# Kernel optimization log

Measured on AMD Instinct MI355X. Metric: run time of the kernel, lower is better.

Reference implementation:

```python
import jax, jax.numpy as jnp
import numpy as np

TOP_K = 2  # config.num_experts_per_tok


def setup_inputs() -> dict:
    key = jax.random.key(0)
    ks = jax.random.split(key, 5)
    B, S, H, F, E = 1, 2048, 2048, 1408, 8
    sc_h = 1.0 / np.sqrt(H)
    sc_f = 1.0 / np.sqrt(F)
    return {
        "hidden_states": jax.random.normal(ks[0], (B, S, H), jnp.float32),
        "gate_w": jax.random.normal(ks[1], (E, H), jnp.float32) * sc_h,
        "w1": jax.random.normal(ks[2], (E, F, H), jnp.float32) * sc_h,
        "w3": jax.random.normal(ks[3], (E, F, H), jnp.float32) * sc_h,
        "w2": jax.random.normal(ks[4], (E, H, F), jnp.float32) * sc_f,
    }


def reference(hidden_states, gate_w, w1, w3, w2):
    B, S, H = hidden_states.shape
    x = hidden_states.reshape(-1, H)            # [T, H]
    T = x.shape[0]
    E = gate_w.shape[0]

    # Router: logits -> fp32 softmax -> top-k -> renormalize
    router_logits = x @ gate_w.T                # [T, E]
    probs = jax.nn.softmax(router_logits.astype(jnp.float32), axis=-1)
    topk_w, topk_idx = jax.lax.top_k(probs, TOP_K)          # [T, K]
    topk_w = topk_w / topk_w.sum(axis=-1, keepdims=True)
    topk_w = topk_w.astype(x.dtype)

    # Scatter top-k weights into a dense [T, E] combine matrix (zero elsewhere)
    w_full = jnp.zeros((T, E), x.dtype).at[jnp.arange(T)[:, None], topk_idx].add(topk_w)

    # Per-expert SwiGLU MLP applied to all tokens; masked combine honors routing.
    g = jnp.einsum('th,efh->etf', x, w1)        # [E, T, F]
    u = jnp.einsum('th,efh->etf', x, w3)        # [E, T, F]
    h = jax.nn.silu(g) * u                      # [E, T, F]
    y = jnp.einsum('etf,ehf->eth', h, w2)       # [E, T, H]
    out = jnp.einsum('eth,te->th', y, w_full)   # [T, H]

    final_hidden_states = out.reshape(B, S, H)
    return final_hidden_states, router_logits
```

## Files before the change

### kernel.cpp

```cpp
#include <hip/hip_runtime.h>
#include <hip/hip_bf16.h>

#define T_TOK 2048
#define H_DIM 2048
#define F_DIM 1408
#define N_EXP 8
#define BM 128
#define BN 64
#define BK 64

#define NITEM 40
#define G1_NY (F_DIM / BN)
#define G2_NY (H_DIM / BN)
#define G1_CHUNK ((NITEM * G1_NY) / 8)
#define G2_CHUNK ((NITEM * G2_NY) / 8)

typedef float f32x4 __attribute__((ext_vector_type(4)));
typedef short s16x8 __attribute__((ext_vector_type(8)));

#define LOFF(row, kbyte) (((row) << 7) + ((kbyte) ^ (((row) & 7) << 4)))

__device__ __forceinline__ int bf2i(__hip_bfloat162 h) {
  int r; __builtin_memcpy(&r, &h, 4); return r;
}

__device__ __forceinline__ int4 pack8(float4 a, float4 b) {
  int4 r;
  r.x = bf2i(__float22bfloat162_rn(float2{a.x, a.y}));
  r.y = bf2i(__float22bfloat162_rn(float2{a.z, a.w}));
  r.z = bf2i(__float22bfloat162_rn(float2{b.x, b.y}));
  r.w = bf2i(__float22bfloat162_rn(float2{b.z, b.w}));
  return r;
}

__device__ __forceinline__ unsigned short f2bf(float f) {
  __hip_bfloat16 h = __float2bfloat16(f);
  unsigned short r; __builtin_memcpy(&r, &h, 2); return r;
}

__device__ __forceinline__ f32x4 mfma16(s16x8 a, s16x8 b, f32x4 c) {
  return __builtin_amdgcn_mfma_f32_16x16x32_bf16(a, b, c, 0, 0, 0);
}

__global__ void router_kernel(const float* __restrict__ x, const float* __restrict__ gw,
                              float* __restrict__ logits, int* __restrict__ tk_idx,
                              float* __restrict__ tk_w, unsigned short* __restrict__ xb) {
  __shared__ float xs[H_DIM];
  __shared__ float lg[N_EXP];
  const int t = blockIdx.x;
  const int tid = threadIdx.x;
  const float4 xv = ((const float4*)(x + (size_t)t * H_DIM))[tid];
  ((float4*)xs)[tid] = xv;
  int2 cw;
  cw.x = bf2i(__float22bfloat162_rn(float2{xv.x, xv.y}));
  cw.y = bf2i(__float22bfloat162_rn(float2{xv.z, xv.w}));
  ((int2*)(xb + (size_t)t * H_DIM))[tid] = cw;
  __syncthreads();
  const int w = tid >> 6, l = tid & 63;
  const float* g = gw + w * H_DIM;
  float s = 0.f;
  for (int j = l; j < H_DIM; j += 64) s += xs[j] * g[j];
#pragma unroll
  for (int o = 32; o; o >>= 1) s += __shfl_down(s, o);
  if (l == 0) lg[w] = s;
  __syncthreads();
  if (tid == 0) {
    float mx = lg[0];
#pragma unroll
    for (int i = 1; i < N_EXP; i++) mx = fmaxf(mx, lg[i]);
    float p[N_EXP];
#pragma unroll
    for (int i = 0; i < N_EXP; i++) p[i] = __expf(lg[i] - mx);
    int i0 = 0;
#pragma unroll
    for (int i = 1; i < N_EXP; i++) if (p[i] > p[i0]) i0 = i;
    int i1 = (i0 == 0) ? 1 : 0;
#pragma unroll
    for (int i = 0; i < N_EXP; i++) if (i != i0 && p[i] > p[i1]) i1 = i;
    const float ww = p[i0] + p[i1];
    tk_idx[t * 2] = i0; tk_idx[t * 2 + 1] = i1;
    tk_w[t * 2] = p[i0] / ww; tk_w[t * 2 + 1] = p[i1] / ww;
#pragma unroll
    for (int i = 0; i < N_EXP; i++) logits[t * N_EXP + i] = lg[i];
  }
}

__global__ void build_lists(const int* __restrict__ tk_idx, const float* __restrict__ tk_w,
                            int* __restrict__ counts, int* __restrict__ entries,
                            float* __restrict__ wlist) {
  const int e = blockIdx.x;
  const int l = threadIdx.x;
  int base = 0;
  for (int t0 = 0; t0 < T_TOK; t0 += 64) {
    const int t = t0 + l;
    int sel = -1; float w = 0.f;
    const int i0 = tk_idx[t * 2], i1 = tk_idx[t * 2 + 1];
    if (i0 == e) { sel = t * 2; w = tk_w[t * 2]; }
    else if (i1 == e) { sel = t * 2 + 1; w = tk_w[t * 2 + 1]; }
    const unsigned long long mask = __ballot(sel >= 0);
    const int pos = base + __popcll(mask & ((1ull << l) - 1ull));
    if (sel >= 0) { entries[e * T_TOK + pos] = sel; wlist[e * T_TOK + pos] = w; }
    base += __popcll(mask);
  }
  if (l == 0) counts[e] = base;
}

__global__ void build_items(const int* __restrict__ counts, int* __restrict__ items) {
  if (threadIdx.x == 0) {
    int n = 0;
#pragma unroll
    for (int e = 0; e < N_EXP; e++) {
      const int c = counts[e];
      for (int m0 = 0; m0 < c; m0 += BM) items[1 + n++] = (e << 16) | (m0 / BM);
    }
    items[0] = n;
  }
}

#define G1_STEP(VA0, VA1, B10, B11, B30, B31, WA0, WA1, WB10, WB11, WB30, WB31, KNEXT) \
  {                                                                           \
    asm volatile("s_waitcnt lgkmcnt(0)" ::: "memory");                        \
    __builtin_amdgcn_s_barrier();                                             \
    *(int4*)(sAc + offA0) = VA0;                                              \
    *(int4*)(sAc + offA1) = VA1;                                              \
    *(int4*)(sB1c + offB) = pack8(B10, B11);                                  \
    *(int4*)(sB3c + offB) = pack8(B30, B31);                                  \
    const int kn = (KNEXT);                                                   \
    WA0 = *(const int4*)(pa0 + kn);                                           \
    WA1 = *(const int4*)(pa1 + kn);                                           \
    WB10 = *(const float4*)(pb1 + kn);                                        \
    WB11 = *(const float4*)(pb1 + kn + 4);                                    \
    WB30 = *(const float4*)(pb3 + kn);                                        \
    WB31 = *(const float4*)(pb3 + kn + 4);                                    \
    asm volatile("s_waitcnt lgkmcnt(0)" ::: "memory");                        \
    __builtin_amdgcn_s_barrier();                                             \
    _Pragma("unroll")                                                         \
    for (int kk = 0; kk < 2; kk++) {                                          \
      const int kbyte = kk * 64 + kb;                                         \
      const s16x8 a0 = *(const s16x8*)(sAc + LOFF(rowA0, kbyte));             \
      const s16x8 a1 = *(const s16x8*)(sAc + LOFF(rowA1, kbyte));             \
      const s16x8 p0 = *(const s16x8*)(sB1c + LOFF(rowB0, kbyte));            \
      const s16x8 p1 = *(const s16x8*)(sB1c + LOFF(rowB1, kbyte));            \
      const s16x8 q0 = *(const s16x8*)(sB3c + LOFF(rowB0, kbyte));            \
      const s16x8 q1 = *(const s16x8*)(sB3c + LOFF(rowB1, kbyte));            \
      aG[0][0] = mfma16(a0, p0, aG[0][0]); aG[0][1] = mfma16(a0, p1, aG[0][1]); \
      aG[1][0] = mfma16(a1, p0, aG[1][0]); aG[1][1] = mfma16(a1, p1, aG[1][1]); \
      aU[0][0] = mfma16(a0, q0, aU[0][0]); aU[0][1] = mfma16(a0, q1, aU[0][1]); \
      aU[1][0] = mfma16(a1, q0, aU[1][0]); aU[1][1] = mfma16(a1, q1, aU[1][1]); \
    }                                                                         \
  }

__global__ __launch_bounds__(512)
void moe_gemm1(const float* __restrict__ w1, const float* __restrict__ w3,
               const unsigned short* __restrict__ xb,
               const int* __restrict__ counts, const int* __restrict__ entries,
               const int* __restrict__ items,
               unsigned short* __restrict__ hb) {
  const int lin = blockIdx.x;
  const int virt = (lin & 7) * G1_CHUNK + (lin >> 3);
  const int ix = virt % NITEM;
  const int iy = virt / NITEM;
  if (ix >= items[0]) return;
  const int it = items[1 + ix];
  const int e = it >> 16;
  const int m0 = (it & 0xffff) * BM;
  const int cnt = counts[e];
  const int rem = cnt - m0;
  const int n0 = iy * BN;

  __shared__ unsigned short sA[BM * BK];
  __shared__ unsigned short sB1[BN * BK];
  __shared__ unsigned short sB3[BN * BK];
  char* sAc = (char*)sA; char* sB1c = (char*)sB1; char* sB3c = (char*)sB3;

  const int tid = threadIdx.x;
  const int lane = tid & 63;
  const int wave = tid >> 6;
  const int wm = wave >> 1, wn = wave & 1;

  const int* elist = entries + e * T_TOK + m0;

  const int r0 = tid >> 3;
  const int gc = tid & 7;
  const int ra1 = r0 + 64;
  const int tok0 = elist[r0 < rem ? r0 : 0] >> 1;
  const int tok1 = elist[ra1 < rem ? ra1 : 0] >> 1;
  const unsigned short* pa0 = xb + (size_t)tok0 * H_DIM + gc * 8;
  const unsigned short* pa1 = xb + (size_t)tok1 * H_DIM + gc * 8;
  const float* pb1 = w1 + ((size_t)e * F_DIM + n0 + r0) * H_DIM + gc * 8;
  const float* pb3 = w3 + ((size_t)e * F_DIM + n0 + r0) * H_DIM + gc * 8;
  const int offA0 = LOFF(r0, gc * 16);
  const int offA1 = LOFF(ra1, gc * 16);
  const int offB = LOFF(r0, gc * 16);

  const int rowA0 = wm * 32 + (lane & 15);
  const int rowA1 = rowA0 + 16;
  const int rowB0 = wn * 32 + (lane & 15);
  const int rowB1 = rowB0 + 16;
  const int kb = (lane >> 4) * 16;

  const f32x4 zero = {0.f, 0.f, 0.f, 0.f};
  f32x4 aG[2][2], aU[2][2];
#pragma unroll
  for (int i = 0; i < 2; i++)
#pragma unroll
    for (int j = 0; j < 2; j++) { aG[i][j] = zero; aU[i][j] = zero; }

  int4 Pa0 = *(const int4*)(pa0), Pa1 = *(const int4*)(pa1);
  float4 Pb10 = *(const float4*)(pb1), Pb11 = *(const float4*)(pb1 + 4);
  float4 Pb30 = *(const float4*)(pb3), Pb31 = *(const float4*)(pb3 + 4);
  int4 Qa0, Qa1;
  float4 Qb10, Qb11, Qb30, Qb31;

  const int NT1 = H_DIM / BK;
  for (int t = 0; t < NT1; t += 2) {
    const int kq = (t + 1 < NT1) ? (t + 1) * BK : 0;
    const int kp = (t + 2 < NT1) ? (t + 2) * BK : 0;
    G1_STEP(Pa0, Pa1, Pb10, Pb11, Pb30, Pb31, Qa0, Qa1, Qb10, Qb11, Qb30, Qb31, kq);
    G1_STEP(Qa0, Qa1, Qb10, Qb11, Qb30, Qb31, Pa0, Pa1, Pb10, Pb11, Pb30, Pb31, kp);
  }

#pragma unroll
  for (int i = 0; i < 2; i++) {
#pragma unroll
    for (int r = 0; r < 4; r++) {
      const int m = wm * 32 + i * 16 + ((lane >> 4) << 2) + r;
      if (m < rem) {
        const int entry = elist[m];
        unsigned short* hp = hb + (size_t)entry * F_DIM + n0 + wn * 32 + (lane & 15);
#pragma unroll
        for (int j = 0; j < 2; j++) {
          const float g = aG[i][j][r];
          const float u = aU[i][j][r];
          const float s = g / (1.f + __expf(-g)) * u;
          hp[j * 16] = f2bf(s);
        }
      }
    }
  }
}

#define G2_STEP(VA0, VA1, B0, B1, WA0, WA1, WB0, WB1, KNEXT)                  \
  {                                                                           \
    asm volatile("s_waitcnt lgkmcnt(0)" ::: "memory");                        \
    __builtin_amdgcn_s_barrier();                                             \
    *(int4*)(sAc + offA0) = VA0;                                              \
    *(int4*)(sAc + offA1) = VA1;                                              \
    *(int4*)(sBc + offB) = pack8(B0, B1);                                     \
    const int kn = (KNEXT);                                                   \
    WA0 = *(const int4*)(pa0 + kn);                                           \
    WA1 = *(const int4*)(pa1 + kn);                                           \
    WB0 = *(const float4*)(pb + kn);                                          \
    WB1 = *(const float4*)(pb + kn + 4);                                      \
    asm volatile("s_waitcnt lgkmcnt(0)" ::: "memory");                        \
    __builtin_amdgcn_s_barrier();                                             \
    _Pragma("unroll")                                                         \
    for (int kk = 0; kk < 2; kk++) {                                          \
      const int kbyte = kk * 64 + kb;                                         \
      const s16x8 a0 = *(const s16x8*)(sAc + LOFF(rowA0, kbyte));             \
      const s16x8 a1 = *(const s16x8*)(sAc + LOFF(rowA1, kbyte));             \
      const s16x8 f0 = *(const s16x8*)(sBc + LOFF(rowB0, kbyte));             \
      const s16x8 f1 = *(const s16x8*)(sBc + LOFF(rowB1, kbyte));             \
      ac[0][0] = mfma16(a0, f0, ac[0][0]); ac[0][1] = mfma16(a0, f1, ac[0][1]); \
      ac[1][0] = mfma16(a1, f0, ac[1][0]); ac[1][1] = mfma16(a1, f1, ac[1][1]); \
    }                                                                         \
  }

__global__ __launch_bounds__(512)
void moe_gemm2(const float* __restrict__ w2,
               const unsigned short* __restrict__ hb,
               const int* __restrict__ counts, const int* __restrict__ entries,
               const float* __restrict__ wlist, const int* __restrict__ items,
               float* __restrict__ out) {
  const int lin = blockIdx.x;
  const int virt = (lin & 7) * G2_CHUNK + (lin >> 3);
  const int ix = virt % NITEM;
  const int iy = virt / NITEM;
  if (ix >= items[0]) return;
  const int it = items[1 + ix];
  const int e = it >> 16;
  const int m0 = (it & 0xffff) * BM;
  const int cnt = counts[e];
  const int rem = cnt - m0;
  const int n0 = iy * BN;

  __shared__ unsigned short sA[BM * BK];
  __shared__ unsigned short sB[BN * BK];
  char* sAc = (char*)sA; char* sBc = (char*)sB;

  const int tid = threadIdx.x;
  const int lane = tid & 63;
  const int wave = tid >> 6;
  const int wm = wave >> 1, wn = wave & 1;

  const int* elist = entries + e * T_TOK + m0;
  const float* wl = wlist + e * T_TOK + m0;

  const int r0 = tid >> 3;
  const int gc = tid & 7;
  const int ra1 = r0 + 64;
  const int en0 = elist[r0 < rem ? r0 : 0];
  const int en1 = elist[ra1 < rem ? ra1 : 0];
  const unsigned short* pa0 = hb + (size_t)en0 * F_DIM + gc * 8;
  const unsigned short* pa1 = hb + (size_t)en1 * F_DIM + gc * 8;
  const float* pb = w2 + ((size_t)e * H_DIM + n0 + r0) * F_DIM + gc * 8;
  const int offA0 = LOFF(r0, gc * 16);
  const int offA1 = LOFF(ra1, gc * 16);
  const int offB = LOFF(r0, gc * 16);

  const int rowA0 = wm * 32 + (lane & 15);
  const int rowA1 = rowA0 + 16;
  const int rowB0 = wn * 32 + (lane & 15);
  const int rowB1 = rowB0 + 16;
  const int kb = (lane >> 4) * 16;

  const f32x4 zero = {0.f, 0.f, 0.f, 0.f};
  f32x4 ac[2][2];
#pragma unroll
  for (int i = 0; i < 2; i++)
#pragma unroll
    for (int j = 0; j < 2; j++) ac[i][j] = zero;

  int4 Pa0 = *(const int4*)(pa0), Pa1 = *(const int4*)(pa1);
  float4 Pb0 = *(const float4*)(pb), Pb1 = *(const float4*)(pb + 4);
  int4 Qa0, Qa1;
  float4 Qb0, Qb1;

  const int NT2 = F_DIM / BK;
  for (int t = 0; t < NT2; t += 2) {
    const int kq = (t + 1 < NT2) ? (t + 1) * BK : 0;
    const int kp = (t + 2 < NT2) ? (t + 2) * BK : 0;
    G2_STEP(Pa0, Pa1, Pb0, Pb1, Qa0, Qa1, Qb0, Qb1, kq);
    G2_STEP(Qa0, Qa1, Qb0, Qb1, Pa0, Pa1, Pb0, Pb1, kp);
  }

#pragma unroll
  for (int i = 0; i < 2; i++) {
#pragma unroll
    for (int r = 0; r < 4; r++) {
      const int m = wm * 32 + i * 16 + ((lane >> 4) << 2) + r;
      if (m < rem) {
        const int entry = elist[m];
        const int t = entry >> 1;
        const float wgt = wl[m];
        float* op = out + (size_t)t * H_DIM + n0 + wn * 32 + (lane & 15);
#pragma unroll
        for (int j = 0; j < 2; j++) atomicAdd(op + j * 16, wgt * ac[i][j][r]);
      }
    }
  }
}

extern "C" void kernel_launch(void* const* d_in, const int* in_sizes, int n_in,
                              void* d_out, int out_size, void* d_ws, size_t ws_size,
                              hipStream_t stream) {
  const float* x  = (const float*)d_in[0];
  const float* gw = (const float*)d_in[1];
  const float* w1 = (const float*)d_in[2];
  const float* w3 = (const float*)d_in[3];
  const float* w2 = (const float*)d_in[4];
  float* out = (float*)d_out;
  float* logits = out + (size_t)T_TOK * H_DIM;

  char* ws = (char*)d_ws;
  size_t off = 0;
  unsigned short* xb = (unsigned short*)(ws + off); off += (size_t)T_TOK * H_DIM * 2;
  unsigned short* hb = (unsigned short*)(ws + off); off += (size_t)T_TOK * 2 * F_DIM * 2;
  int*   tk_idx = (int*)(ws + off);   off += (size_t)T_TOK * 2 * 4;
  float* tk_w   = (float*)(ws + off); off += (size_t)T_TOK * 2 * 4;
  int*   counts = (int*)(ws + off);   off += 256;
  int*   entries = (int*)(ws + off);  off += (size_t)N_EXP * T_TOK * 4;
  float* wlist  = (float*)(ws + off); off += (size_t)N_EXP * T_TOK * 4;
  int*   items  = (int*)(ws + off);   off += 256;

  (void)hipMemsetAsync(d_out, 0, (size_t)out_size * sizeof(float), stream);
  router_kernel<<<dim3(T_TOK), 512, 0, stream>>>(x, gw, logits, tk_idx, tk_w, xb);
  build_lists<<<dim3(N_EXP), 64, 0, stream>>>(tk_idx, tk_w, counts, entries, wlist);
  build_items<<<dim3(1), 64, 0, stream>>>(counts, items);
  moe_gemm1<<<dim3(NITEM * G1_NY), 512, 0, stream>>>(w1, w3, xb, counts, entries, items, hb);
  moe_gemm2<<<dim3(NITEM * G2_NY), 512, 0, stream>>>(w2, hb, counts, entries, wlist, items, out);
}
```

Measured before the change: 246.1 us.

## Load gathered A tiles directly into LDS with double-buffered async DMA

Both MoE GEMM kernels now fetch the gathered bf16 activation tiles with global_load_lds, which writes straight into a double-buffered shared-memory A tile and skips the register staging path. The swizzle is folded into the global column offset. The fp32 weight loads are prefetched two K-steps ahead, and vmcnt waits let the weight loads stay in flight across barriers. This is meant to cut VGPR pressure and LDS store instructions and to deepen the memory pipeline, at the cost of extra LDS for the second A buffer and fragile waitcnt bookkeeping.

```diff
diff --git a/kernel.cpp b/kernel.cpp
--- a/kernel.cpp
+++ b/kernel.cpp
@@ -17,6 +17,7 @@
 
 typedef float f32x4 __attribute__((ext_vector_type(4)));
 typedef short s16x8 __attribute__((ext_vector_type(8)));
+typedef unsigned int u32;
 
 #define LOFF(row, kbyte) (((row) << 7) + ((kbyte) ^ (((row) & 7) << 4)))
 
@@ -40,6 +41,11 @@
 
 __device__ __forceinline__ f32x4 mfma16(s16x8 a, s16x8 b, f32x4 c) {
   return __builtin_amdgcn_mfma_f32_16x16x32_bf16(a, b, c, 0, 0, 0);
+}
+
+__device__ __forceinline__ void dma16(const unsigned short* g, unsigned short* l) {
+  __builtin_amdgcn_global_load_lds((const __attribute__((address_space(1))) u32*)g,
+                                   (__attribute__((address_space(3))) u32*)l, 16, 0, 0);
 }
 
 __global__ void router_kernel(const float* __restrict__ x, const float* __restrict__ gw,
@@ -117,28 +123,31 @@
   }
 }
 
-#define G1_STEP(VA0, VA1, B10, B11, B30, B31, WA0, WA1, WB10, WB11, WB30, WB31, KNEXT) \
+#define G1_STEP(SARD, SAWR, RB1, RB3, KA1_, KB2_)                             \
   {                                                                           \
-    asm volatile("s_waitcnt lgkmcnt(0)" ::: "memory");                        \
+    asm volatile("s_waitcnt vmcnt(4) lgkmcnt(0)" ::: "memory");               \
     __builtin_amdgcn_s_barrier();                                             \
-    *(int4*)(sAc + offA0) = VA0;                                              \
-    *(int4*)(sAc + offA1) = VA1;                                              \
-    *(int4*)(sB1c + offB) = pack8(B10, B11);                                  \
-    *(int4*)(sB3c + offB) = pack8(B30, B31);                                  \
-    const int kn = (KNEXT);                                                   \
-    WA0 = *(const int4*)(pa0 + kn);                                           \
-    WA1 = *(const int4*)(pa1 + kn);                                           \
-    WB10 = *(const float4*)(pb1 + kn);                                        \
-    WB11 = *(const float4*)(pb1 + kn + 4);                                    \
-    WB30 = *(const float4*)(pb3 + kn);                                        \
-    WB31 = *(const float4*)(pb3 + kn + 4);                                    \
+    *(int4*)(sB1c + offB) = pack8(RB1[0], RB1[1]);                            \
+    *(int4*)(sB3c + offB) = pack8(RB3[0], RB3[1]);                            \
+    {                                                                         \
+      const int ka = (KA1_);                                                  \
+      dma16(ga0 + ka, (SAWR) + aw);                                           \
+      dma16(ga1 + ka, (SAWR) + aw + 512);                                     \
+    }                                                                         \
+    {                                                                         \
+      const int kbl = (KB2_);                                                 \
+      RB1[0] = *(const float4*)(pb1 + kbl);                                   \
+      RB1[1] = *(const float4*)(pb1 + kbl + 4);                               \
+      RB3[0] = *(const float4*)(pb3 + kbl);                                   \
+      RB3[1] = *(const float4*)(pb3 + kbl + 4);                               \
+    }                                                                         \
     asm volatile("s_waitcnt lgkmcnt(0)" ::: "memory");                        \
     __builtin_amdgcn_s_barrier();                                             \
     _Pragma("unroll")                                                         \
     for (int kk = 0; kk < 2; kk++) {                                          \
       const int kbyte = kk * 64 + kb;                                         \
-      const s16x8 a0 = *(const s16x8*)(sAc + LOFF(rowA0, kbyte));             \
-      const s16x8 a1 = *(const s16x8*)(sAc + LOFF(rowA1, kbyte));             \
+      const s16x8 a0 = *(const s16x8*)((const char*)(SARD) + LOFF(rowA0, kbyte)); \
+      const s16x8 a1 = *(const s16x8*)((const char*)(SARD) + LOFF(rowA1, kbyte)); \
       const s16x8 p0 = *(const s16x8*)(sB1c + LOFF(rowB0, kbyte));            \
       const s16x8 p1 = *(const s16x8*)(sB1c + LOFF(rowB1, kbyte));            \
       const s16x8 q0 = *(const s16x8*)(sB3c + LOFF(rowB0, kbyte));            \
@@ -164,14 +173,13 @@
   const int it = items[1 + ix];
   const int e = it >> 16;
   const int m0 = (it & 0xffff) * BM;
-  const int cnt = counts[e];
-  const int rem = cnt - m0;
+  const int rem = counts[e] - m0;
   const int n0 = iy * BN;
 
-  __shared__ unsigned short sA[BM * BK];
+  __shared__ unsigned short sA[2][BM * BK];
   __shared__ unsigned short sB1[BN * BK];
   __shared__ unsigned short sB3[BN * BK];
-  char* sAc = (char*)sA; char* sB1c = (char*)sB1; char* sB3c = (char*)sB3;
+  char* sB1c = (char*)sB1; char* sB3c = (char*)sB3;
 
   const int tid = threadIdx.x;
   const int lane = tid & 63;
@@ -182,16 +190,18 @@
 
   const int r0 = tid >> 3;
   const int gc = tid & 7;
-  const int ra1 = r0 + 64;
-  const int tok0 = elist[r0 < rem ? r0 : 0] >> 1;
-  const int tok1 = elist[ra1 < rem ? ra1 : 0] >> 1;
-  const unsigned short* pa0 = xb + (size_t)tok0 * H_DIM + gc * 8;
-  const unsigned short* pa1 = xb + (size_t)tok1 * H_DIM + gc * 8;
   const float* pb1 = w1 + ((size_t)e * F_DIM + n0 + r0) * H_DIM + gc * 8;
   const float* pb3 = w3 + ((size_t)e * F_DIM + n0 + r0) * H_DIM + gc * 8;
-  const int offA0 = LOFF(r0, gc * 16);
-  const int offA1 = LOFF(ra1, gc * 16);
   const int offB = LOFF(r0, gc * 16);
+
+  const int arow0 = wave * 16 + (lane >> 3);
+  const int arow1 = arow0 + 8;
+  const int gcolb = (((lane & 7) << 4) ^ (((lane >> 3) & 7) << 4));
+  const int tokA0 = elist[arow0 < rem ? arow0 : 0] >> 1;
+  const int tokA1 = elist[arow1 < rem ? arow1 : 0] >> 1;
+  const unsigned short* ga0 = xb + (size_t)tokA0 * H_DIM + (gcolb >> 1);
+  const unsigned short* ga1 = xb + (size_t)tokA1 * H_DIM + (gcolb >> 1);
+  const int aw = wave * 1024;
 
   const int rowA0 = wm * 32 + (lane & 15);
   const int rowA1 = rowA0 + 16;
@@ -206,18 +216,22 @@
 #pragma unroll
     for (int j = 0; j < 2; j++) { aG[i][j] = zero; aU[i][j] = zero; }
 
-  int4 Pa0 = *(const int4*)(pa0), Pa1 = *(const int4*)(pa1);
-  float4 Pb10 = *(const float4*)(pb1), Pb11 = *(const float4*)(pb1 + 4);
-  float4 Pb30 = *(const float4*)(pb3), Pb31 = *(const float4*)(pb3 + 4);
-  int4 Qa0, Qa1;
-  float4 Qb10, Qb11, Qb30, Qb31;
-
-  const int NT1 = H_DIM / BK;
-  for (int t = 0; t < NT1; t += 2) {
-    const int kq = (t + 1 < NT1) ? (t + 1) * BK : 0;
-    const int kp = (t + 2 < NT1) ? (t + 2) * BK : 0;
-    G1_STEP(Pa0, Pa1, Pb10, Pb11, Pb30, Pb31, Qa0, Qa1, Qb10, Qb11, Qb30, Qb31, kq);
-    G1_STEP(Qa0, Qa1, Qb10, Qb11, Qb30, Qb31, Pa0, Pa1, Pb10, Pb11, Pb30, Pb31, kp);
+  dma16(ga0, sA[0] + aw);
+  dma16(ga1, sA[0] + aw + 512);
+  float4 P1[2], P3[2], Q1[2], Q3[2];
+  P1[0] = *(const float4*)(pb1);      P1[1] = *(const float4*)(pb1 + 4);
+  P3[0] = *(const float4*)(pb3);      P3[1] = *(const float4*)(pb3 + 4);
+  Q1[0] = *(const float4*)(pb1 + BK); Q1[1] = *(const float4*)(pb1 + BK + 4);
+  Q3[0] = *(const float4*)(pb3 + BK); Q3[1] = *(const float4*)(pb3 + BK + 4);
+
+  const int NT = H_DIM / BK;
+  for (int t = 0; t < NT; t += 2) {
+    const int ka1 = (t + 1 < NT) ? (t + 1) * BK : 0;
+    const int ka2 = (t + 2 < NT) ? (t + 2) * BK : 0;
+    const int kb2 = ka2;
+    const int kb3 = (t + 3 < NT) ? (t + 3) * BK : 0;
+    G1_STEP(sA[0], sA[1], P1, P3, ka1, kb2);
+    G1_STEP(sA[1], sA[0], Q1, Q3, ka2, kb3);
   }
 
 #pragma unroll
@@ -232,33 +246,35 @@
         for (int j = 0; j < 2; j++) {
           const float g = aG[i][j][r];
           const float u = aU[i][j][r];
-          const float s = g / (1.f + __expf(-g)) * u;
-          hp[j * 16] = f2bf(s);
+          hp[j * 16] = f2bf(g / (1.f + __expf(-g)) * u);
         }
       }
     }
   }
 }
 
-#define G2_STEP(VA0, VA1, B0, B1, WA0, WA1, WB0, WB1, KNEXT)                  \
+#define G2_STEP(SARD, SAWR, RB, KA1_, KB2_)                                   \
   {                                                                           \
-    asm volatile("s_waitcnt lgkmcnt(0)" ::: "memory");                        \
+    asm volatile("s_waitcnt vmcnt(2) lgkmcnt(0)" ::: "memory");               \
     __builtin_amdgcn_s_barrier();                                             \
-    *(int4*)(sAc + offA0) = VA0;                                              \
-    *(int4*)(sAc + offA1) = VA1;                                              \
-    *(int4*)(sBc + offB) = pack8(B0, B1);                                     \
-    const int kn = (KNEXT);                                                   \
-    WA0 = *(const int4*)(pa0 + kn);                                           \
-    WA1 = *(const int4*)(pa1 + kn);                                           \
-    WB0 = *(const float4*)(pb + kn);                                          \
-    WB1 = *(const float4*)(pb + kn + 4);                                      \
+    *(int4*)(sBc + offB) = pack8(RB[0], RB[1]);                               \
+    {                                                                         \
+      const int ka = (KA1_);                                                  \
+      dma16(ga0 + ka, (SAWR) + aw);                                           \
+      dma16(ga1 + ka, (SAWR) + aw + 512);                                     \
+    }                                                                         \
+    {                                                                         \
+      const int kbl = (KB2_);                                                 \
+      RB[0] = *(const float4*)(pb + kbl);                                     \
+      RB[1] = *(const float4*)(pb + kbl + 4);                                 \
+    }                                                                         \
     asm volatile("s_waitcnt lgkmcnt(0)" ::: "memory");                        \
     __builtin_amdgcn_s_barrier();                                             \
     _Pragma("unroll")                                                         \
     for (int kk = 0; kk < 2; kk++) {                                          \
       const int kbyte = kk * 64 + kb;                                         \
-      const s16x8 a0 = *(const s16x8*)(sAc + LOFF(rowA0, kbyte));             \
-      const s16x8 a1 = *(const s16x8*)(sAc + LOFF(rowA1, kbyte));             \
+      const s16x8 a0 = *(const s16x8*)((const char*)(SARD) + LOFF(rowA0, kbyte)); \
+      const s16x8 a1 = *(const s16x8*)((const char*)(SARD) + LOFF(rowA1, kbyte)); \
       const s16x8 f0 = *(const s16x8*)(sBc + LOFF(rowB0, kbyte));             \
       const s16x8 f1 = *(const s16x8*)(sBc + LOFF(rowB1, kbyte));             \
       ac[0][0] = mfma16(a0, f0, ac[0][0]); ac[0][1] = mfma16(a0, f1, ac[0][1]); \
@@ -280,13 +296,12 @@
   const int it = items[1 + ix];
   const int e = it >> 16;
   const int m0 = (it & 0xffff) * BM;
-  const int cnt = counts[e];
-  const int rem = cnt - m0;
+  const int rem = counts[e] - m0;
   const int n0 = iy * BN;
 
-  __shared__ unsigned short sA[BM * BK];
+  __shared__ unsigned short sA[2][BM * BK];
   __shared__ unsigned short sB[BN * BK];
-  char* sAc = (char*)sA; char* sBc = (char*)sB;
+  char* sBc = (char*)sB;
 
   const int tid = threadIdx.x;
   const int lane = tid & 63;
@@ -298,15 +313,17 @@
 
   const int r0 = tid >> 3;
   const int gc = tid & 7;
-  const int ra1 = r0 + 64;
-  const int en0 = elist[r0 < rem ? r0 : 0];
-  const int en1 = elist[ra1 < rem ? ra1 : 0];
-  const unsigned short* pa0 = hb + (size_t)en0 * F_DIM + gc * 8;
-  const unsigned short* pa1 = hb + (size_t)en1 * F_DIM + gc * 8;
   const float* pb = w2 + ((size_t)e * H_DIM + n0 + r0) * F_DIM + gc * 8;
-  const int offA0 = LOFF(r0, gc * 16);
-  const int offA1 = LOFF(ra1, gc * 16);
   const int offB = LOFF(r0, gc * 16);
+
+  const int arow0 = wave * 16 + (lane >> 3);
+  const int arow1 = arow0 + 8;
+  const int gcolb = (((lane & 7) << 4) ^ (((lane >> 3) & 7) << 4));
+  const int enA0 = elist[arow0 < rem ? arow0 : 0];
+  const int enA1 = elist[arow1 < rem ? arow1 : 0];
+  const unsigned short* ga0 = hb + (size_t)enA0 * F_DIM + (gcolb >> 1);
+  const unsigned short* ga1 = hb + (size_t)enA1 * F_DIM + (gcolb >> 1);
+  const int aw = wave * 1024;
 
   const int rowA0 = wm * 32 + (lane & 15);
   const int rowA1 = rowA0 + 16;
@@ -321,17 +338,20 @@
 #pragma unroll
     for (int j = 0; j < 2; j++) ac[i][j] = zero;
 
-  int4 Pa0 = *(const int4*)(pa0), Pa1 = *(const int4*)(pa1);
-  float4 Pb0 = *(const float4*)(pb), Pb1 = *(const float4*)(pb + 4);
-  int4 Qa0, Qa1;
-  float4 Qb0, Qb1;
-
-  const int NT2 = F_DIM / BK;
-  for (int t = 0; t < NT2; t += 2) {
-    const int kq = (t + 1 < NT2) ? (t + 1) * BK : 0;
-    const int kp = (t + 2 < NT2) ? (t + 2) * BK : 0;
-    G2_STEP(Pa0, Pa1, Pb0, Pb1, Qa0, Qa1, Qb0, Qb1, kq);
-    G2_STEP(Qa0, Qa1, Qb0, Qb1, Pa0, Pa1, Pb0, Pb1, kp);
+  dma16(ga0, sA[0] + aw);
+  dma16(ga1, sA[0] + aw + 512);
+  float4 P[2], Q[2];
+  P[0] = *(const float4*)(pb);      P[1] = *(const float4*)(pb + 4);
+  Q[0] = *(const float4*)(pb + BK); Q[1] = *(const float4*)(pb + BK + 4);
+
+  const int NT = F_DIM / BK;
+  for (int t = 0; t < NT; t += 2) {
+    const int ka1 = (t + 1 < NT) ? (t + 1) * BK : 0;
+    const int ka2 = (t + 2 < NT) ? (t + 2) * BK : 0;
+    const int kb2 = ka2;
+    const int kb3 = (t + 3 < NT) ? (t + 3) * BK : 0;
+    G2_STEP(sA[0], sA[1], P, ka1, kb2);
+    G2_STEP(sA[1], sA[0], Q, ka2, kb3);
   }
 
 #pragma unroll
@@ -341,9 +361,9 @@
       const int m = wm * 32 + i * 16 + ((lane >> 4) << 2) + r;
       if (m < rem) {
         const int entry = elist[m];
-        const int t = entry >> 1;
+        const int tok = entry >> 1;
         const float wgt = wl[m];
-        float* op = out + (size_t)t * H_DIM + n0 + wn * 32 + (lane & 15);
+        float* op = out + (size_t)tok * H_DIM + n0 + wn * 32 + (lane & 15);
 #pragma unroll
         for (int j = 0; j < 2; j++) atomicAdd(op + j * 16, wgt * ac[i][j][r]);
       }
```

Result: faster. 233.6 us (-5.1%).
